# Kernel tuning notes

Hardware: AMD Instinct MI355X
Metric: run time of the kernel (lower is better)

## Reference

```python
import jax, jax.numpy as jnp
import numpy as np

S, B, N, DIM = 64, 4, 256, 256
HEADS, DIM_HEAD = 8, 32
INNER = HEADS * DIM_HEAD  # 256
SCALE = DIM_HEAD ** -0.5
NEG = -1e10


def setup_inputs() -> dict:
    key = jax.random.key(0)
    k1, k2, k3, k4, k5 = jax.random.split(key, 5)
    x = jax.random.normal(k1, (S, B, N, DIM), dtype=jnp.float32)
    mask = jax.random.randint(k2, (S, N, N), 0, 2, dtype=jnp.int32)
    # nn.Linear(dim, inner*3, bias=False): y = x @ W_qkv  (W stored transposed)
    W_qkv = jax.random.normal(k3, (DIM, 3 * INNER), dtype=jnp.float32) / np.sqrt(DIM)
    W_out = jax.random.normal(k4, (INNER, DIM), dtype=jnp.float32) / np.sqrt(INNER)
    b_out = jax.random.normal(k5, (DIM,), dtype=jnp.float32) * 0.01
    return {"x": x, "mask": mask, "W_qkv": W_qkv, "W_out": W_out, "b_out": b_out}


def reference(x, mask, W_qkv, W_out, b_out):
    s, b, n, _ = x.shape
    qkv = x @ W_qkv                                  # [s,b,n,3*inner]
    q, k, v = jnp.split(qkv, 3, axis=-1)
    def to_heads(t):
        # s b n (h d) -> s b h n d
        return t.reshape(s, b, n, HEADS, DIM_HEAD).transpose(0, 1, 3, 2, 4)
    q, k, v = to_heads(q), to_heads(k), to_heads(v)
    sim = jnp.einsum('sbhid,sbhjd->sbhij', q, k) * SCALE
    sim = jnp.where(mask[:, None, None, :, :] == 0, NEG, sim)
    attn = jax.nn.softmax(sim, axis=-1)
    out = jnp.einsum('sbhij,sbhjd->sbhid', attn, v)
    out = out.transpose(0, 1, 3, 2, 4).reshape(s, b, n, INNER)  # s b h n d -> s b n (h d)
    return out @ W_out + b_out
```

## Files before the change

kernel.cpp:

```cpp
#include <hip/hip_runtime.h>

typedef __attribute__((ext_vector_type(8))) short bf16x8;
typedef __attribute__((ext_vector_type(4))) float f32x4;

__device__ __forceinline__ unsigned short f2bf(float f) {
  unsigned int u = __builtin_bit_cast(unsigned int, f);
  u += 0x7fffu + ((u >> 16) & 1u);
  return (unsigned short)(u >> 16);
}

typedef const __attribute__((address_space(1))) unsigned int* as1_u32p;
typedef __attribute__((address_space(3))) unsigned int* as3_u32p;
__device__ __forceinline__ void glds16(const void* g, void* l) {
  __builtin_amdgcn_global_load_lds((as1_u32p)g, (as3_u32p)l, 16, 0, 0);
}

__global__ __launch_bounds__(256) void cvt_kernel(const float* __restrict__ X,
                                                  unsigned short* __restrict__ Y) {
  const long long i = ((long long)blockIdx.x * 256 + threadIdx.x) * 8;
  float4 a = *reinterpret_cast<const float4*>(X + i);
  float4 b = *reinterpret_cast<const float4*>(X + i + 4);
  bf16x8 t;
  t[0] = (short)f2bf(a.x); t[1] = (short)f2bf(a.y);
  t[2] = (short)f2bf(a.z); t[3] = (short)f2bf(a.w);
  t[4] = (short)f2bf(b.x); t[5] = (short)f2bf(b.y);
  t[6] = (short)f2bf(b.z); t[7] = (short)f2bf(b.w);
  *reinterpret_cast<bf16x8*>(Y + i) = t;
}

__global__ __launch_bounds__(256) void transpose_bf16_kernel(
    const float* __restrict__ S, unsigned short* __restrict__ D, int R, int C) {
  __shared__ float T[32][33];
  const int bx = blockIdx.x * 32;
  const int by = blockIdx.y * 32;
  const int tx = threadIdx.x & 31, ty = threadIdx.x >> 5;
#pragma unroll
  for (int k = 0; k < 4; ++k)
    T[ty + 8 * k][tx] = S[(size_t)(by + ty + 8 * k) * C + bx + tx];
  __syncthreads();
#pragma unroll
  for (int k = 0; k < 4; ++k)
    D[(size_t)(bx + ty + 8 * k) * R + by + tx] = f2bf(T[tx][ty + 8 * k]);
}

__global__ __launch_bounds__(256) void pack_mask_kernel(const int* __restrict__ mask,
                                                        unsigned short* __restrict__ Mb) {
  const int t = blockIdx.x * 256 + threadIdx.x;
  const int l = t & 15;
  const int r = t >> 4;
  const int* mp = mask + ((size_t)r << 8) + l;
  unsigned int bits = 0;
#pragma unroll
  for (int ct = 0; ct < 16; ++ct)
    bits |= (mp[ct << 4] != 0 ? (1u << ct) : 0u);
  Mb[t] = (unsigned short)bits;
}

template <bool C_F32>
__global__ __launch_bounds__(256) void gemm_bt(
    const unsigned short* __restrict__ A,
    const unsigned short* __restrict__ Bt,
    void* __restrict__ Cv,
    const float* __restrict__ bias,
    int M, int N, int K)
{
  __shared__ __align__(16) unsigned short As[128 * 32];
  __shared__ __align__(16) unsigned short Bs[128 * 32];

  const int tid  = threadIdx.x;
  const int bm   = blockIdx.x * 128;
  const int bn   = blockIdx.y * 128;
  const int lane = tid & 63;
  const int wave = tid >> 6;
  const int wr   = (wave >> 1) * 64;
  const int wc   = (wave & 1) * 64;
  const int l15  = lane & 15;
  const int quad = lane >> 4;

  f32x4 acc[4][4];
#pragma unroll
  for (int r = 0; r < 4; ++r)
#pragma unroll
    for (int c = 0; c < 4; ++c) {
      f32x4 z = {0.f, 0.f, 0.f, 0.f};
      acc[r][c] = z;
    }

  const unsigned short* gA0 = A  + (size_t)(bm + wave * 16 + (lane >> 2)) * K + (lane & 3) * 8;
  const unsigned short* gA1 = gA0 + (size_t)64 * K;
  const unsigned short* gB0 = Bt + (size_t)(bn + wave * 16 + (lane >> 2)) * K + (lane & 3) * 8;
  const unsigned short* gB1 = gB0 + (size_t)64 * K;
  unsigned short* lA0 = As + wave * 512;
  unsigned short* lA1 = As + 2048 + wave * 512;
  unsigned short* lB0 = Bs + wave * 512;
  unsigned short* lB1 = Bs + 2048 + wave * 512;

  for (int kk = 0; kk < K; kk += 32) {
    glds16(gA0 + kk, lA0);
    glds16(gA1 + kk, lA1);
    glds16(gB0 + kk, lB0);
    glds16(gB1 + kk, lB1);
    __syncthreads();

    bf16x8 af[4], bf[4];
#pragma unroll
    for (int i = 0; i < 4; ++i) {
      af[i] = *reinterpret_cast<const bf16x8*>(&As[(wr + i * 16 + l15) * 32 + quad * 8]);
      bf[i] = *reinterpret_cast<const bf16x8*>(&Bs[(wc + i * 16 + l15) * 32 + quad * 8]);
    }
#pragma unroll
    for (int rt = 0; rt < 4; ++rt)
#pragma unroll
      for (int ct = 0; ct < 4; ++ct)
        acc[rt][ct] = __builtin_amdgcn_mfma_f32_16x16x32_bf16(af[rt], bf[ct], acc[rt][ct], 0, 0, 0);
    __syncthreads();
  }

#pragma unroll
  for (int rt = 0; rt < 4; ++rt)
#pragma unroll
    for (int ct = 0; ct < 4; ++ct)
#pragma unroll
      for (int i = 0; i < 4; ++i) {
        const int row = bm + wr + rt * 16 + quad * 4 + i;
        const int col = bn + wc + ct * 16 + l15;
        const float v = acc[rt][ct][i];
        if constexpr (C_F32) {
          ((float*)Cv)[(size_t)row * N + col] = v + bias[col];
        } else {
          ((unsigned short*)Cv)[(size_t)row * N + col] = f2bf(v);
        }
      }
}

#define SCALE_F 0.17677669529663689f

__global__ __launch_bounds__(256) void attn_kernel(
    const unsigned short* __restrict__ QKV,
    const unsigned short* __restrict__ Mb,
    unsigned short* __restrict__ Aout)
{
  __shared__ __align__(16) unsigned short Ks[256 * 32];
  __shared__ __align__(16) unsigned short SH[4 * 16 * 280];

  const int blk  = blockIdx.x;
  const int h    = blk & 7;
  const int sb   = blk >> 3;
  const int s    = sb >> 2;
  const int t0   = sb << 8;
  const int tid  = threadIdx.x;
  const int lane = tid & 63;
  const int wave = tid >> 6;
  const int l15  = lane & 15;
  const int quad = lane >> 4;

  {
    const unsigned short* kp = QKV + (size_t)(t0 + tid) * 768 + 256 + h * 32;
    const unsigned short* vp = kp + 256;
    const int sw = (tid >> 1) & 3;
    unsigned short* kd = Ks + tid * 32;
    unsigned short* vd = SH + tid * 38;
#pragma unroll
    for (int g = 0; g < 4; ++g)
      *reinterpret_cast<uint4*>(kd + ((g ^ sw) << 3)) = *reinterpret_cast<const uint4*>(kp + g * 8);
#pragma unroll
    for (int i = 0; i < 16; ++i)
      *reinterpret_cast<unsigned int*>(vd + i * 2) = *reinterpret_cast<const unsigned int*>(vp + i * 2);
  }
  __syncthreads();

  bf16x8 bv[2][8];
#pragma unroll
  for (int dt = 0; dt < 2; ++dt)
#pragma unroll
    for (int ks = 0; ks < 8; ++ks) {
      bf16x8 v;
#pragma unroll
      for (int j = 0; j < 8; ++j)
        v[j] = (short)SH[(ks * 32 + quad * 8 + j) * 38 + dt * 16 + l15];
      bv[dt][ks] = v;
    }
  __syncthreads();

  unsigned short* P = SH + wave * (16 * 280);
  const int swr = (l15 >> 1) & 3;

  for (int qb = 0; qb < 4; ++qb) {
    const int qbase = wave * 64 + qb * 16;

    bf16x8 qf = *reinterpret_cast<const bf16x8*>(
        QKV + (size_t)(t0 + qbase + l15) * 768 + h * 32 + quad * 8);

    unsigned short mbits[4];
#pragma unroll
    for (int i = 0; i < 4; ++i)
      mbits[i] = Mb[(((size_t)s << 12)) + ((size_t)(qbase + quad * 4 + i) << 4) + l15];

    f32x4 sim[16];
#pragma unroll
    for (int ct = 0; ct < 16; ++ct) {
      bf16x8 kf = *reinterpret_cast<const bf16x8*>(
          &Ks[(ct * 16 + l15) * 32 + ((quad ^ swr) << 3)]);
      f32x4 z = {0.f, 0.f, 0.f, 0.f};
      sim[ct] = __builtin_amdgcn_mfma_f32_16x16x32_bf16(qf, kf, z, 0, 0, 0);
    }

    float lsum[4];
#pragma unroll
    for (int i = 0; i < 4; ++i) {
      const unsigned int mw = mbits[i];
      float mx = -3.0e38f;
#pragma unroll
      for (int ct = 0; ct < 16; ++ct) {
        float v = sim[ct][i] * SCALE_F;
        if (!((mw >> ct) & 1u)) v = -1.0e10f;
        sim[ct][i] = v;
        mx = fmaxf(mx, v);
      }
#pragma unroll
      for (int off = 1; off < 16; off <<= 1)
        mx = fmaxf(mx, __shfl_xor(mx, off, 64));
      float sum = 0.f;
#pragma unroll
      for (int ct = 0; ct < 16; ++ct) {
        float e = __expf(sim[ct][i] - mx);
        sim[ct][i] = e;
        sum += e;
      }
#pragma unroll
      for (int off = 1; off < 16; off <<= 1)
        sum += __shfl_xor(sum, off, 64);
      lsum[i] = sum;
    }

#pragma unroll
    for (int i = 0; i < 4; ++i)
#pragma unroll
      for (int ct = 0; ct < 16; ++ct)
        P[(quad * 4 + i) * 280 + ct * 16 + l15] = f2bf(sim[ct][i]);
    __syncthreads();

    f32x4 o0 = {0.f, 0.f, 0.f, 0.f};
    f32x4 o1 = {0.f, 0.f, 0.f, 0.f};
#pragma unroll
    for (int ks = 0; ks < 8; ++ks) {
      bf16x8 pf = *reinterpret_cast<const bf16x8*>(&P[l15 * 280 + ks * 32 + quad * 8]);
      o0 = __builtin_amdgcn_mfma_f32_16x16x32_bf16(pf, bv[0][ks], o0, 0, 0, 0);
      o1 = __builtin_amdgcn_mfma_f32_16x16x32_bf16(pf, bv[1][ks], o1, 0, 0, 0);
    }

#pragma unroll
    for (int i = 0; i < 4; ++i) {
      const float rl = 1.0f / lsum[i];
      const size_t row = (size_t)t0 + qbase + quad * 4 + i;
      Aout[row * 256 + h * 32 + l15]      = f2bf(o0[i] * rl);
      Aout[row * 256 + h * 32 + 16 + l15] = f2bf(o1[i] * rl);
    }
    __syncthreads();
  }
}

extern "C" void kernel_launch(void* const* d_in, const int* in_sizes, int n_in,
                              void* d_out, int out_size, void* d_ws, size_t ws_size,
                              hipStream_t stream) {
  const float* X    = (const float*)d_in[0];
  const int*   mask = (const int*)d_in[1];
  const float* Wqkv = (const float*)d_in[2];
  const float* Wout = (const float*)d_in[3];
  const float* bout = (const float*)d_in[4];
  float*       outp = (float*)d_out;

  unsigned short* QKV   = (unsigned short*)d_ws;
  unsigned short* Xbf   = QKV + (size_t)65536 * 768;
  unsigned short* Amid  = Xbf;
  unsigned short* WoutT = QKV;
  unsigned short* WqkvT = (unsigned short*)d_out;
  unsigned short* Mbits = (unsigned short*)d_out + ((size_t)16 << 20);

  dim3 blk(256);
  cvt_kernel<<<dim3(8192), blk, 0, stream>>>(X, Xbf);
  transpose_bf16_kernel<<<dim3(24, 8), blk, 0, stream>>>(Wqkv, WqkvT, 256, 768);
  pack_mask_kernel<<<dim3(1024), blk, 0, stream>>>(mask, Mbits);

  gemm_bt<false><<<dim3(512, 6), blk, 0, stream>>>(Xbf, WqkvT, (void*)QKV, nullptr, 65536, 768, 256);
  attn_kernel<<<dim3(2048), blk, 0, stream>>>(QKV, Mbits, Amid);

  transpose_bf16_kernel<<<dim3(8, 8), blk, 0, stream>>>(Wout, WoutT, 256, 256);
  gemm_bt<true><<<dim3(512, 2), blk, 0, stream>>>(Amid, WoutT, (void*)outp, bout, 65536, 256, 256);
}
```

Measured before the change: 301.1 us.

## Keep softmax probabilities in registers, double-buffer GEMM LDS, ballot-pack mask

The attention kernel now computes the transposed score tile (K·Q), so each lane owns one query column. Its softmax reductions need only two cross-lane shuffles, and the probabilities are packed to bf16 in registers and fed straight into the PV MFMA. This removes the LDS round trip for P and the per-query-block barriers. The GEMM gets a two-stage LDS double buffer so the next K-tile's global-to-LDS loads overlap the MFMAs. The mask packing now uses wave ballots into 32-bit words, and V staging is re-laid to match the new operand order. The changes add more LDS use in the GEMM and the register pressure of keeping P in registers.

Measured after the change: 311.4 us. +3.4%, slower.

```diff
diff --git a/kernel.cpp b/kernel.cpp
--- a/kernel.cpp
+++ b/kernel.cpp
@@ -7,6 +7,12 @@
   unsigned int u = __builtin_bit_cast(unsigned int, f);
   u += 0x7fffu + ((u >> 16) & 1u);
   return (unsigned short)(u >> 16);
+}
+
+__device__ __forceinline__ unsigned int cvt_pk_bf16(float lo, float hi) {
+  unsigned int r;
+  asm("v_cvt_pk_bf16_f32 %0, %1, %2" : "=v"(r) : "v"(lo), "v"(hi));
+  return r;
 }
 
 typedef const __attribute__((address_space(1))) unsigned int* as1_u32p;
@@ -44,16 +50,12 @@
 }
 
 __global__ __launch_bounds__(256) void pack_mask_kernel(const int* __restrict__ mask,
-                                                        unsigned short* __restrict__ Mb) {
-  const int t = blockIdx.x * 256 + threadIdx.x;
-  const int l = t & 15;
-  const int r = t >> 4;
-  const int* mp = mask + ((size_t)r << 8) + l;
-  unsigned int bits = 0;
-#pragma unroll
-  for (int ct = 0; ct < 16; ++ct)
-    bits |= (mp[ct << 4] != 0 ? (1u << ct) : 0u);
-  Mb[t] = (unsigned short)bits;
+                                                        unsigned int* __restrict__ Mb) {
+  const int g = blockIdx.x * 256 + threadIdx.x;
+  const unsigned long long bal = __ballot(mask[g] != 0);
+  const int lane = threadIdx.x & 63;
+  if ((lane & 31) == 0)
+    Mb[g >> 5] = (unsigned int)(bal >> (lane & 32));
 }
 
 template <bool C_F32>
@@ -64,8 +66,8 @@
     const float* __restrict__ bias,
     int M, int N, int K)
 {
-  __shared__ __align__(16) unsigned short As[128 * 32];
-  __shared__ __align__(16) unsigned short Bs[128 * 32];
+  __shared__ __align__(16) unsigned short As[2][128 * 32];
+  __shared__ __align__(16) unsigned short Bs[2][128 * 32];
 
   const int tid  = threadIdx.x;
   const int bm   = blockIdx.x * 128;
@@ -90,23 +92,31 @@
   const unsigned short* gA1 = gA0 + (size_t)64 * K;
   const unsigned short* gB0 = Bt + (size_t)(bn + wave * 16 + (lane >> 2)) * K + (lane & 3) * 8;
   const unsigned short* gB1 = gB0 + (size_t)64 * K;
-  unsigned short* lA0 = As + wave * 512;
-  unsigned short* lA1 = As + 2048 + wave * 512;
-  unsigned short* lB0 = Bs + wave * 512;
-  unsigned short* lB1 = Bs + 2048 + wave * 512;
-
-  for (int kk = 0; kk < K; kk += 32) {
-    glds16(gA0 + kk, lA0);
-    glds16(gA1 + kk, lA1);
-    glds16(gB0 + kk, lB0);
-    glds16(gB1 + kk, lB1);
-    __syncthreads();
-
+  const int woff = wave * 512;
+
+  glds16(gA0, &As[0][woff]);
+  glds16(gA1, &As[0][2048 + woff]);
+  glds16(gB0, &Bs[0][woff]);
+  glds16(gB1, &Bs[0][2048 + woff]);
+  __syncthreads();
+
+  const int nt = K >> 5;
+  for (int t = 0; t < nt; ++t) {
+    const int cur = t & 1;
+    if (t + 1 < nt) {
+      const int kk = (t + 1) << 5;
+      unsigned short* an = As[cur ^ 1];
+      unsigned short* bn_ = Bs[cur ^ 1];
+      glds16(gA0 + kk, an + woff);
+      glds16(gA1 + kk, an + 2048 + woff);
+      glds16(gB0 + kk, bn_ + woff);
+      glds16(gB1 + kk, bn_ + 2048 + woff);
+    }
     bf16x8 af[4], bf[4];
 #pragma unroll
     for (int i = 0; i < 4; ++i) {
-      af[i] = *reinterpret_cast<const bf16x8*>(&As[(wr + i * 16 + l15) * 32 + quad * 8]);
-      bf[i] = *reinterpret_cast<const bf16x8*>(&Bs[(wc + i * 16 + l15) * 32 + quad * 8]);
+      af[i] = *reinterpret_cast<const bf16x8*>(&As[cur][(wr + i * 16 + l15) * 32 + quad * 8]);
+      bf[i] = *reinterpret_cast<const bf16x8*>(&Bs[cur][(wc + i * 16 + l15) * 32 + quad * 8]);
     }
 #pragma unroll
     for (int rt = 0; rt < 4; ++rt)
@@ -137,11 +147,11 @@
 
 __global__ __launch_bounds__(256) void attn_kernel(
     const unsigned short* __restrict__ QKV,
-    const unsigned short* __restrict__ Mb,
+    const unsigned int* __restrict__ Mb,
     unsigned short* __restrict__ Aout)
 {
   __shared__ __align__(16) unsigned short Ks[256 * 32];
-  __shared__ __align__(16) unsigned short SH[4 * 16 * 280];
+  __shared__ __align__(16) unsigned short Vs[256 * 36];
 
   const int blk  = blockIdx.x;
   const int h    = blk & 7;
@@ -159,7 +169,7 @@
     const unsigned short* vp = kp + 256;
     const int sw = (tid >> 1) & 3;
     unsigned short* kd = Ks + tid * 32;
-    unsigned short* vd = SH + tid * 38;
+    unsigned short* vd = Vs + tid * 36;
 #pragma unroll
     for (int g = 0; g < 4; ++g)
       *reinterpret_cast<uint4*>(kd + ((g ^ sw) << 3)) = *reinterpret_cast<const uint4*>(kp + g * 8);
@@ -173,16 +183,16 @@
 #pragma unroll
   for (int dt = 0; dt < 2; ++dt)
 #pragma unroll
-    for (int ks = 0; ks < 8; ++ks) {
+    for (int c = 0; c < 8; ++c) {
       bf16x8 v;
 #pragma unroll
-      for (int j = 0; j < 8; ++j)
-        v[j] = (short)SH[(ks * 32 + quad * 8 + j) * 38 + dt * 16 + l15];
-      bv[dt][ks] = v;
-    }
-  __syncthreads();
-
-  unsigned short* P = SH + wave * (16 * 280);
+      for (int j = 0; j < 8; ++j) {
+        const int row = c * 32 + ((j < 4) ? (quad * 4 + j) : (16 + quad * 4 + (j - 4)));
+        v[j] = (short)Vs[row * 36 + dt * 16 + l15];
+      }
+      bv[dt][c] = v;
+    }
+
   const int swr = (l15 >> 1) & 3;
 
   for (int qb = 0; qb < 4; ++qb) {
@@ -191,10 +201,15 @@
     bf16x8 qf = *reinterpret_cast<const bf16x8*>(
         QKV + (size_t)(t0 + qbase + l15) * 768 + h * 32 + quad * 8);
 
-    unsigned short mbits[4];
-#pragma unroll
-    for (int i = 0; i < 4; ++i)
-      mbits[i] = Mb[(((size_t)s << 12)) + ((size_t)(qbase + quad * 4 + i) << 4) + l15];
+    unsigned int msk[8];
+    {
+      const unsigned int* mrow = Mb + (((size_t)s * 256 + qbase + l15) << 3);
+      uint4 m0 = *reinterpret_cast<const uint4*>(mrow);
+      uint4 m1 = *reinterpret_cast<const uint4*>(mrow + 4);
+      const int qs = quad * 4;
+      msk[0] = m0.x >> qs; msk[1] = m0.y >> qs; msk[2] = m0.z >> qs; msk[3] = m0.w >> qs;
+      msk[4] = m1.x >> qs; msk[5] = m1.y >> qs; msk[6] = m1.z >> qs; msk[7] = m1.w >> qs;
+    }
 
     f32x4 sim[16];
 #pragma unroll
@@ -202,61 +217,55 @@
       bf16x8 kf = *reinterpret_cast<const bf16x8*>(
           &Ks[(ct * 16 + l15) * 32 + ((quad ^ swr) << 3)]);
       f32x4 z = {0.f, 0.f, 0.f, 0.f};
-      sim[ct] = __builtin_amdgcn_mfma_f32_16x16x32_bf16(qf, kf, z, 0, 0, 0);
-    }
-
-    float lsum[4];
-#pragma unroll
-    for (int i = 0; i < 4; ++i) {
-      const unsigned int mw = mbits[i];
-      float mx = -3.0e38f;
-#pragma unroll
-      for (int ct = 0; ct < 16; ++ct) {
+      sim[ct] = __builtin_amdgcn_mfma_f32_16x16x32_bf16(kf, qf, z, 0, 0, 0);
+    }
+
+    float mx = -3.0e38f;
+#pragma unroll
+    for (int ct = 0; ct < 16; ++ct)
+#pragma unroll
+      for (int i = 0; i < 4; ++i) {
         float v = sim[ct][i] * SCALE_F;
-        if (!((mw >> ct) & 1u)) v = -1.0e10f;
+        if (!((msk[ct >> 1] >> ((ct & 1) * 16 + i)) & 1u)) v = -1.0e10f;
         sim[ct][i] = v;
         mx = fmaxf(mx, v);
       }
-#pragma unroll
-      for (int off = 1; off < 16; off <<= 1)
-        mx = fmaxf(mx, __shfl_xor(mx, off, 64));
-      float sum = 0.f;
-#pragma unroll
-      for (int ct = 0; ct < 16; ++ct) {
+    mx = fmaxf(mx, __shfl_xor(mx, 16, 64));
+    mx = fmaxf(mx, __shfl_xor(mx, 32, 64));
+
+    float sum = 0.f;
+#pragma unroll
+    for (int ct = 0; ct < 16; ++ct)
+#pragma unroll
+      for (int i = 0; i < 4; ++i) {
         float e = __expf(sim[ct][i] - mx);
         sim[ct][i] = e;
         sum += e;
       }
-#pragma unroll
-      for (int off = 1; off < 16; off <<= 1)
-        sum += __shfl_xor(sum, off, 64);
-      lsum[i] = sum;
-    }
-
-#pragma unroll
-    for (int i = 0; i < 4; ++i)
-#pragma unroll
-      for (int ct = 0; ct < 16; ++ct)
-        P[(quad * 4 + i) * 280 + ct * 16 + l15] = f2bf(sim[ct][i]);
-    __syncthreads();
+    sum += __shfl_xor(sum, 16, 64);
+    sum += __shfl_xor(sum, 32, 64);
+    const float rl = 1.0f / sum;
 
     f32x4 o0 = {0.f, 0.f, 0.f, 0.f};
     f32x4 o1 = {0.f, 0.f, 0.f, 0.f};
 #pragma unroll
-    for (int ks = 0; ks < 8; ++ks) {
-      bf16x8 pf = *reinterpret_cast<const bf16x8*>(&P[l15 * 280 + ks * 32 + quad * 8]);
-      o0 = __builtin_amdgcn_mfma_f32_16x16x32_bf16(pf, bv[0][ks], o0, 0, 0, 0);
-      o1 = __builtin_amdgcn_mfma_f32_16x16x32_bf16(pf, bv[1][ks], o1, 0, 0, 0);
+    for (int c = 0; c < 8; ++c) {
+      uint4 u;
+      u.x = cvt_pk_bf16(sim[2 * c][0] * rl,     sim[2 * c][1] * rl);
+      u.y = cvt_pk_bf16(sim[2 * c][2] * rl,     sim[2 * c][3] * rl);
+      u.z = cvt_pk_bf16(sim[2 * c + 1][0] * rl, sim[2 * c + 1][1] * rl);
+      u.w = cvt_pk_bf16(sim[2 * c + 1][2] * rl, sim[2 * c + 1][3] * rl);
+      bf16x8 pf = __builtin_bit_cast(bf16x8, u);
+      o0 = __builtin_amdgcn_mfma_f32_16x16x32_bf16(pf, bv[0][c], o0, 0, 0, 0);
+      o1 = __builtin_amdgcn_mfma_f32_16x16x32_bf16(pf, bv[1][c], o1, 0, 0, 0);
     }
 
 #pragma unroll
     for (int i = 0; i < 4; ++i) {
-      const float rl = 1.0f / lsum[i];
       const size_t row = (size_t)t0 + qbase + quad * 4 + i;
-      Aout[row * 256 + h * 32 + l15]      = f2bf(o0[i] * rl);
-      Aout[row * 256 + h * 32 + 16 + l15] = f2bf(o1[i] * rl);
-    }
-    __syncthreads();
+      Aout[row * 256 + h * 32 + l15]      = f2bf(o0[i]);
+      Aout[row * 256 + h * 32 + 16 + l15] = f2bf(o1[i]);
+    }
   }
 }
 
@@ -275,12 +284,12 @@
   unsigned short* Amid  = Xbf;
   unsigned short* WoutT = QKV;
   unsigned short* WqkvT = (unsigned short*)d_out;
-  unsigned short* Mbits = (unsigned short*)d_out + ((size_t)16 << 20);
+  unsigned int*   Mbits = (unsigned int*)((char*)d_out + ((size_t)32 << 20));
 
   dim3 blk(256);
   cvt_kernel<<<dim3(8192), blk, 0, stream>>>(X, Xbf);
   transpose_bf16_kernel<<<dim3(24, 8), blk, 0, stream>>>(Wqkv, WqkvT, 256, 768);
-  pack_mask_kernel<<<dim3(1024), blk, 0, stream>>>(mask, Mbits);
+  pack_mask_kernel<<<dim3(16384), blk, 0, stream>>>(mask, Mbits);
 
   gemm_bt<false><<<dim3(512, 6), blk, 0, stream>>>(Xbf, WqkvT, (void*)QKV, nullptr, 65536, 768, 256);
   attn_kernel<<<dim3(2048), blk, 0, stream>>>(QKV, Mbits, Amid);
```
